# Kernel optimization log

Measured on AMD Instinct MI355X. Metric: run time of the kernel, lower is better.

## Reference

```python
import jax, jax.numpy as jnp
import numpy as np

S, B, D, H, A = 1024, 256, 128, 256, 256  # seq, batch, input_dim, hidden_dim, attention_dim


def setup_inputs() -> dict:
    key = jax.random.key(0)
    ks = jax.random.split(key, 8)
    sc_in = 1.0 / np.sqrt(D + H)
    sc_h = 1.0 / np.sqrt(H)
    inp = {
        "inputs": jax.random.normal(ks[0], (S, B, D), dtype=jnp.float32),
        "mask": jnp.ones((S, B), dtype=jnp.int32),
        "Wf": jax.random.uniform(ks[1], (D + H, H), jnp.float32, -sc_in, sc_in),
        "bf": jnp.zeros((H,), jnp.float32),
        "Wi": jax.random.uniform(ks[2], (D + H, H), jnp.float32, -sc_in, sc_in),
        "bi": jnp.zeros((H,), jnp.float32),
        "Wg": jax.random.uniform(ks[3], (D + H, H), jnp.float32, -sc_in, sc_in),
        "bg": jnp.zeros((H,), jnp.float32),
        "Wo": jax.random.uniform(ks[4], (D + H, H), jnp.float32, -sc_in, sc_in),
        "bo": jnp.zeros((H,), jnp.float32),
        "Wa": jax.random.uniform(ks[5], (H, A), jnp.float32, -sc_h, sc_h),
        "ba": jnp.zeros((A,), jnp.float32),
    }
    return inp


def reference(inputs, mask, Wf, bf, Wi, bi, Wg, bg, Wo, bo, Wa, ba):
    seq_len, batch, _ = inputs.shape
    h0 = jnp.zeros((batch, H), inputs.dtype)
    c0 = jnp.zeros((batch, H), inputs.dtype)
    mask_f = mask.astype(inputs.dtype)[:, :, None]  # (S, B, 1)

    def step(carry, xm):
        hx, cx = carry
        x_t, m_t = xm  # (B, D), (B, 1)
        combined = jnp.concatenate([x_t, hx], axis=1)  # (B, D+H)
        f = jax.nn.sigmoid(combined @ Wf + bf)
        i = jax.nn.sigmoid(combined @ Wi + bi)
        g = jnp.tanh(combined @ Wg + bg)
        o = jax.nn.sigmoid(combined @ Wo + bo)
        # masked gates: forget/output default to 1, input/update to 0 on padding
        f = f * m_t + (1.0 - m_t)
        i = i * m_t
        g = g * m_t
        o = o * m_t + (1.0 - m_t)
        cx = f * cx + i * g
        hx = o * jnp.tanh(cx)
        return (hx, cx), hx

    (hx, cx), outputs = jax.lax.scan(step, (h0, c0), (inputs, mask_f))  # outputs (S, B, H)

    # attention pooling over the time axis (dim 0); attention_dim == hidden_dim
    attn_weights = jax.nn.softmax(outputs @ Wa + ba, axis=0)  # (S, B, A)
    context = jnp.sum(attn_weights * outputs, axis=0)  # (B, H)
    outputs = jnp.broadcast_to(context[None, :, :], (seq_len, batch, H))
    return outputs, (hx, cx)
```

## Files before the change

### kernel.cpp

```cpp
#include <hip/hip_runtime.h>
#include <cstdint>
#include <cstddef>

#define WS_WHP   0
#define WS_WXP   524288
#define WS_WAP   786432
#define WS_CTX   917504
#define WS_XPROJ 1179648

typedef _Float16 h2_t __attribute__((ext_vector_type(2)));

static __device__ __forceinline__ float fdot2(uint32_t a, uint32_t b, float acc) {
#if __has_builtin(__builtin_amdgcn_fdot2)
    return __builtin_amdgcn_fdot2(__builtin_bit_cast(h2_t, a),
                                  __builtin_bit_cast(h2_t, b), acc, false);
#else
    union { uint32_t u; _Float16 f[2]; } ua, ub;
    ua.u = a; ub.u = b;
    return acc + (float)ua.f[0] * (float)ub.f[0] + (float)ua.f[1] * (float)ub.f[1];
#endif
}

static __device__ __forceinline__ uint32_t packh2(float x, float y) {
    h2_t v; v[0] = (_Float16)x; v[1] = (_Float16)y;
    return __builtin_bit_cast(uint32_t, v);
}
static __device__ __forceinline__ uint16_t f16b(float v) {
    _Float16 h = (_Float16)v; return __builtin_bit_cast(uint16_t, h);
}
static __device__ __forceinline__ float h16tof(uint16_t u) {
    return (float)__builtin_bit_cast(_Float16, u);
}
static __device__ __forceinline__ float sigm(float x) {
    return 1.0f / (1.0f + __expf(-x));
}
static __device__ __forceinline__ float tanh_fast(float x) {
    float ax = fabsf(x);
    float e = __expf(-2.0f * ax);
    float r = (1.0f - e) / (1.0f + e);
    return (x < 0.0f) ? -r : r;
}

__global__ void k_pack(const float* __restrict__ Wf, const float* __restrict__ Wi,
                       const float* __restrict__ Wg2, const float* __restrict__ Wo,
                       const float* __restrict__ Wa,
                       uint32_t* __restrict__ whp, uint32_t* __restrict__ wxp,
                       uint32_t* __restrict__ wap) {
    int idx = blockIdx.x * 256 + threadIdx.x;
    if (idx < 131072) {
        int p = idx >> 10, c = idx & 1023;
        int g = c >> 8, u = c & 255;
        const float* W = (g == 0) ? Wf : (g == 1) ? Wi : (g == 2) ? Wg2 : Wo;
        whp[idx] = packh2(W[(128 + 2 * p) * 256 + u], W[(129 + 2 * p) * 256 + u]);
    } else if (idx < 196608) {
        int j = idx - 131072;
        int p = j >> 10, c = j & 1023;
        int g = c >> 8, u = c & 255;
        const float* W = (g == 0) ? Wf : (g == 1) ? Wi : (g == 2) ? Wg2 : Wo;
        wxp[j] = packh2(W[(2 * p) * 256 + u], W[(2 * p + 1) * 256 + u]);
    } else if (idx < 229376) {
        int j = idx - 196608;
        int p = j >> 8, aa = j & 255;
        wap[j] = packh2(Wa[(2 * p) * 256 + aa], Wa[(2 * p + 1) * 256 + aa]);
    }
}

__global__ __launch_bounds__(512) void k_xproj(
        const float* __restrict__ x,
        const float* __restrict__ bfp, const float* __restrict__ bip,
        const float* __restrict__ bgp, const float* __restrict__ bop,
        const uint32_t* __restrict__ wxp, uint16_t* __restrict__ xproj) {
    __shared__ uint32_t xs[512];
    int t = threadIdx.x;
    int c0 = t, c1 = t + 512;
    uint32_t wx0[64], wx1[64];
#pragma unroll
    for (int p = 0; p < 64; ++p) {
        wx0[p] = wxp[p * 1024 + c0];
        wx1[p] = wxp[p * 1024 + c1];
    }
    float bias0 = (t < 256) ? bfp[t] : bip[t - 256];
    float bias1 = (t < 256) ? bgp[t] : bop[t - 256];
    int srow = t >> 6, pp = t & 63;
    long row0 = (long)blockIdx.x * 128;
    for (int ch = 0; ch < 16; ++ch) {
        long rbase = row0 + ch * 8;
        const float2* xr = (const float2*)(x + (rbase + srow) * 128) + pp;
        float2 xv = *xr;
        __syncthreads();
        xs[srow * 64 + pp] = packh2(xv.x, xv.y);
        __syncthreads();
#pragma unroll 1
        for (int r = 0; r < 8; ++r) {
            const uint32_t* hrow = xs + r * 64;
            float a0 = 0.f, d0 = 0.f, a1 = 0.f, d1 = 0.f;
#pragma unroll
            for (int p = 0; p < 64; p += 4) {
                uint4 hv = *(const uint4*)(hrow + p);
                a0 = fdot2(wx0[p + 0], hv.x, a0); d0 = fdot2(wx0[p + 1], hv.y, d0);
                a0 = fdot2(wx0[p + 2], hv.z, a0); d0 = fdot2(wx0[p + 3], hv.w, d0);
                a1 = fdot2(wx1[p + 0], hv.x, a1); d1 = fdot2(wx1[p + 1], hv.y, d1);
                a1 = fdot2(wx1[p + 2], hv.z, a1); d1 = fdot2(wx1[p + 3], hv.w, d1);
            }
            size_t orow = (size_t)(rbase + r) * 1024;
            xproj[orow + c0] = f16b(a0 + d0 + bias0);
            xproj[orow + c1] = f16b(a1 + d1 + bias1);
        }
    }
}

#define RECUR_LDS 152064

__global__ __launch_bounds__(512, 2) void k_recur(
        const uint32_t* __restrict__ whp, const uint16_t* __restrict__ xproj,
        const int* __restrict__ mask, uint16_t* __restrict__ oseq,
        float* __restrict__ dout) {
    extern __shared__ uint32_t smem[];
    uint32_t* wlds = smem;
    uint32_t* h2   = smem + 36864;
    float*    P    = (float*)(smem + 36992);
    int t = threadIdx.x;
    int b = blockIdx.x;
    int c0 = t, c1 = t + 512;

    for (int j = t; j < 32768; j += 512) {
        int c = j >> 5, pp = j & 31;
        wlds[c * 36 + pp] = whp[(96 + pp) * 1024 + c];
    }
    if (t < 128) h2[t] = 0u;

    uint32_t w0[96], w1[96];
#pragma unroll
    for (int p = 0; p < 96; ++p) {
        w0[p] = whp[p * 1024 + c0];
        w1[p] = whp[p * 1024 + c1];
    }
    float c_state = 0.f, h_state = 0.f;
    const uint16_t* xp_ptr = xproj + b * 1024;
    uint16_t* oseq_ptr = oseq + b * 256;
    uint16_t xv0 = xp_ptr[c0], xv1 = xp_ptr[c1];
    int mv = mask[b];
    __syncthreads();

    for (int s = 0; s < 1024; ++s) {
        float xpf0 = h16tof(xv0), xpf1 = h16tof(xv1);
        float mcur = (float)mv;
        xp_ptr += 262144;
        if (s < 1023) {
            xv0 = xp_ptr[c0]; xv1 = xp_ptr[c1];
            mv = mask[(s + 1) * 256 + b];
        }
        float a0 = 0.f, b0 = 0.f, a1 = 0.f, b1 = 0.f;
#pragma unroll
        for (int j = 0; j < 8; ++j) {
            uint4 hv = *(const uint4*)(h2 + 96 + j * 4);
            uint4 wA = *(const uint4*)(wlds + c0 * 36 + j * 4);
            uint4 wB = *(const uint4*)(wlds + c1 * 36 + j * 4);
            a0 = fdot2(wA.x, hv.x, a0); b0 = fdot2(wA.y, hv.y, b0);
            a0 = fdot2(wA.z, hv.z, a0); b0 = fdot2(wA.w, hv.w, b0);
            a1 = fdot2(wB.x, hv.x, a1); b1 = fdot2(wB.y, hv.y, b1);
            a1 = fdot2(wB.z, hv.z, a1); b1 = fdot2(wB.w, hv.w, b1);
        }
#pragma unroll
        for (int j = 0; j < 24; ++j) {
            uint4 hv = *(const uint4*)(h2 + j * 4);
            a0 = fdot2(w0[4 * j + 0], hv.x, a0); b0 = fdot2(w0[4 * j + 1], hv.y, b0);
            a0 = fdot2(w0[4 * j + 2], hv.z, a0); b0 = fdot2(w0[4 * j + 3], hv.w, b0);
            a1 = fdot2(w1[4 * j + 0], hv.x, a1); b1 = fdot2(w1[4 * j + 1], hv.y, b1);
            a1 = fdot2(w1[4 * j + 2], hv.z, a1); b1 = fdot2(w1[4 * j + 3], hv.w, b1);
        }
        P[c0] = a0 + b0 + xpf0;
        P[c1] = a1 + b1 + xpf1;
        __syncthreads();
        if (t < 256) {
            float fg = sigm(P[t]);
            float ig = sigm(P[256 + t]);
            float gg = tanh_fast(P[512 + t]);
            float og = sigm(P[768 + t]);
            fg = fg * mcur + (1.0f - mcur);
            ig = ig * mcur;
            gg = gg * mcur;
            og = og * mcur + (1.0f - mcur);
            c_state = fg * c_state + ig * gg;
            h_state = og * tanh_fast(c_state);
            uint16_t hb = f16b(h_state);
            ((uint16_t*)h2)[t] = hb;
            oseq_ptr[t] = hb;
        }
        __syncthreads();
        oseq_ptr += 65536;
    }
    if (t < 256) {
        dout[67108864 + b * 256 + t] = h_state;
        dout[67174400 + b * 256 + t] = c_state;
    }
}

__global__ __launch_bounds__(256) void k_attn(
        const uint32_t* __restrict__ wap, const float* __restrict__ ba,
        const uint16_t* __restrict__ oseq, float* __restrict__ ctx) {
    __shared__ uint32_t rb[2][128];
    int a = threadIdx.x, b = blockIdx.x;
    uint32_t wa[128];
#pragma unroll
    for (int p = 0; p < 128; ++p) wa[p] = wap[p * 256 + a];
    float bias = ba[a];
    const uint32_t* orow = (const uint32_t*)oseq + b * 128;
    if (a < 128) rb[0][a] = orow[a];
    __syncthreads();
    float m = -3.0e38f, Z = 0.f, acc = 0.f;
    for (int s = 0; s < 1024; ++s) {
        uint32_t nxt = 0;
        if (s < 1023 && a < 128) nxt = orow[32768 * (s + 1) + a];
        const uint32_t* row = rb[s & 1];
        float l0 = bias, l1 = 0.f, l2 = 0.f, l3 = 0.f;
#pragma unroll
        for (int p = 0; p < 128; p += 4) {
            uint4 hv = *(const uint4*)(row + p);
            l0 = fdot2(wa[p + 0], hv.x, l0);
            l1 = fdot2(wa[p + 1], hv.y, l1);
            l2 = fdot2(wa[p + 2], hv.z, l2);
            l3 = fdot2(wa[p + 3], hv.w, l3);
        }
        float l = (l0 + l1) + (l2 + l3);
        uint32_t pv = row[a >> 1];
        float hself = h16tof((a & 1) ? (uint16_t)(pv >> 16) : (uint16_t)(pv & 0xffffu));
        float m2 = fmaxf(m, l);
        float al = __expf(m - m2);
        float pr = __expf(l - m2);
        Z = Z * al + pr;
        acc = acc * al + pr * hself;
        m = m2;
        if (s < 1023 && a < 128) rb[(s + 1) & 1][a] = nxt;
        __syncthreads();
    }
    ctx[b * 256 + a] = acc / Z;
}

__global__ void k_bcast(const float4* __restrict__ ctx4, float4* __restrict__ out4) {
    int i = blockIdx.x * 256 + threadIdx.x;
    out4[i] = ctx4[i & 16383];
}

extern "C" void kernel_launch(void* const* d_in, const int* in_sizes, int n_in,
                              void* d_out, int out_size, void* d_ws, size_t ws_size,
                              hipStream_t stream) {
    const float* x    = (const float*)d_in[0];
    const int*   mask = (const int*)d_in[1];
    const float* Wf   = (const float*)d_in[2];
    const float* bf   = (const float*)d_in[3];
    const float* Wi   = (const float*)d_in[4];
    const float* bi   = (const float*)d_in[5];
    const float* Wg   = (const float*)d_in[6];
    const float* bg   = (const float*)d_in[7];
    const float* Wo   = (const float*)d_in[8];
    const float* bo   = (const float*)d_in[9];
    const float* Wa   = (const float*)d_in[10];
    const float* ba   = (const float*)d_in[11];
    float* out = (float*)d_out;
    char*  ws  = (char*)d_ws;

    uint32_t* whp   = (uint32_t*)(ws + WS_WHP);
    uint32_t* wxp   = (uint32_t*)(ws + WS_WXP);
    uint32_t* wap   = (uint32_t*)(ws + WS_WAP);
    float*    ctx   = (float*)(ws + WS_CTX);
    uint16_t* xproj = (uint16_t*)(ws + WS_XPROJ);
    uint16_t* oseq  = (uint16_t*)d_out;

    (void)in_sizes; (void)n_in; (void)out_size; (void)ws_size;

    hipFuncSetAttribute((const void*)k_recur,
                        hipFuncAttributeMaxDynamicSharedMemorySize, RECUR_LDS);

    k_pack<<<896, 256, 0, stream>>>(Wf, Wi, Wg, Wo, Wa, whp, wxp, wap);
    k_xproj<<<2048, 512, 0, stream>>>(x, bf, bi, bg, bo, wxp, xproj);
    k_recur<<<256, 512, RECUR_LDS, stream>>>(whp, xproj, mask, oseq, out);
    k_attn<<<256, 256, 0, stream>>>(wap, ba, oseq, ctx);
    k_bcast<<<65536, 256, 0, stream>>>((const float4*)ctx, (float4*)out);
}
```

Baseline: 3.866 ms.

## Restructure LSTM recurrence to one thread per hidden unit, split attention over time

The recurrent kernel now uses 256 threads, each computing all four gates for one hidden unit. Weights are split between registers (400 per thread) and LDS, and the hidden state is double-buffered, which removes one of the two barriers per step and the gate-exchange through shared memory. The attention pooling is split into four time chunks per batch, with partial max/sum/accumulator results merged by a new small kernel, so more blocks run in parallel. Risks are high register pressure from the 400-element weight arrays, which may cause spills, and fewer threads per CU during the serial recurrence.

```diff
diff --git a/kernel.cpp b/kernel.cpp
--- a/kernel.cpp
+++ b/kernel.cpp
@@ -109,109 +109,113 @@
     }
 }
 
-#define RECUR_LDS 152064
-
-__global__ __launch_bounds__(512, 2) void k_recur(
+#define RECUR_LDS 115712
+
+__global__ __launch_bounds__(256, 1) void k_recur(
         const uint32_t* __restrict__ whp, const uint16_t* __restrict__ xproj,
         const int* __restrict__ mask, uint16_t* __restrict__ oseq,
         float* __restrict__ dout) {
     extern __shared__ uint32_t smem[];
-    uint32_t* wlds = smem;
-    uint32_t* h2   = smem + 36864;
-    float*    P    = (float*)(smem + 36992);
+    uint32_t* wlds  = smem;
+    uint32_t* hbuf0 = smem + 28672;
+    uint32_t* hbuf1 = smem + 28800;
     int t = threadIdx.x;
     int b = blockIdx.x;
-    int c0 = t, c1 = t + 512;
-
-    for (int j = t; j < 32768; j += 512) {
-        int c = j >> 5, pp = j & 31;
-        wlds[c * 36 + pp] = whp[(96 + pp) * 1024 + c];
-    }
-    if (t < 128) h2[t] = 0u;
-
-    uint32_t w0[96], w1[96];
-#pragma unroll
-    for (int p = 0; p < 96; ++p) {
-        w0[p] = whp[p * 1024 + c0];
-        w1[p] = whp[p * 1024 + c1];
+
+    for (int p = 0; p < 28; ++p)
+        for (int c = t; c < 1024; c += 256)
+            wlds[c * 28 + p] = whp[(100 + p) * 1024 + c];
+    if (t < 128) hbuf0[t] = 0u;
+
+    uint32_t w0[100], w1[100], w2[100], w3[100];
+#pragma unroll
+    for (int p = 0; p < 100; ++p) {
+        const uint32_t* r = whp + p * 1024 + t;
+        w0[p] = r[0]; w1[p] = r[256]; w2[p] = r[512]; w3[p] = r[768];
     }
     float c_state = 0.f, h_state = 0.f;
-    const uint16_t* xp_ptr = xproj + b * 1024;
-    uint16_t* oseq_ptr = oseq + b * 256;
-    uint16_t xv0 = xp_ptr[c0], xv1 = xp_ptr[c1];
+    const uint16_t* xp = xproj + b * 1024 + t;
+    uint16_t* op = oseq + b * 256 + t;
+    uint16_t xf = xp[0], xi = xp[256], xg = xp[512], xo = xp[768];
     int mv = mask[b];
+    const uint32_t* wl = wlds + t * 28;
     __syncthreads();
 
     for (int s = 0; s < 1024; ++s) {
-        float xpf0 = h16tof(xv0), xpf1 = h16tof(xv1);
+        const uint32_t* hb = (s & 1) ? hbuf1 : hbuf0;
+        uint32_t*       hn = (s & 1) ? hbuf0 : hbuf1;
+        float pf = h16tof(xf), pi = h16tof(xi), pg = h16tof(xg), po = h16tof(xo);
         float mcur = (float)mv;
-        xp_ptr += 262144;
+        xp += 262144;
         if (s < 1023) {
-            xv0 = xp_ptr[c0]; xv1 = xp_ptr[c1];
+            xf = xp[0]; xi = xp[256]; xg = xp[512]; xo = xp[768];
             mv = mask[(s + 1) * 256 + b];
         }
-        float a0 = 0.f, b0 = 0.f, a1 = 0.f, b1 = 0.f;
-#pragma unroll
-        for (int j = 0; j < 8; ++j) {
-            uint4 hv = *(const uint4*)(h2 + 96 + j * 4);
-            uint4 wA = *(const uint4*)(wlds + c0 * 36 + j * 4);
-            uint4 wB = *(const uint4*)(wlds + c1 * 36 + j * 4);
-            a0 = fdot2(wA.x, hv.x, a0); b0 = fdot2(wA.y, hv.y, b0);
-            a0 = fdot2(wA.z, hv.z, a0); b0 = fdot2(wA.w, hv.w, b0);
-            a1 = fdot2(wB.x, hv.x, a1); b1 = fdot2(wB.y, hv.y, b1);
-            a1 = fdot2(wB.z, hv.z, a1); b1 = fdot2(wB.w, hv.w, b1);
-        }
-#pragma unroll
-        for (int j = 0; j < 24; ++j) {
-            uint4 hv = *(const uint4*)(h2 + j * 4);
-            a0 = fdot2(w0[4 * j + 0], hv.x, a0); b0 = fdot2(w0[4 * j + 1], hv.y, b0);
-            a0 = fdot2(w0[4 * j + 2], hv.z, a0); b0 = fdot2(w0[4 * j + 3], hv.w, b0);
-            a1 = fdot2(w1[4 * j + 0], hv.x, a1); b1 = fdot2(w1[4 * j + 1], hv.y, b1);
-            a1 = fdot2(w1[4 * j + 2], hv.z, a1); b1 = fdot2(w1[4 * j + 3], hv.w, b1);
-        }
-        P[c0] = a0 + b0 + xpf0;
-        P[c1] = a1 + b1 + xpf1;
+        float f0 = 0.f, f1 = 0.f, i0 = 0.f, i1 = 0.f;
+        float g0 = 0.f, g1 = 0.f, o0 = 0.f, o1 = 0.f;
+#pragma unroll
+        for (int j = 0; j < 7; ++j) {
+            uint4 hv = *(const uint4*)(hb + 100 + 4 * j);
+            uint4 wa = *(const uint4*)(wl + 4 * j);
+            uint4 wb = *(const uint4*)(wl + 7168 + 4 * j);
+            uint4 wc = *(const uint4*)(wl + 14336 + 4 * j);
+            uint4 wd = *(const uint4*)(wl + 21504 + 4 * j);
+            f0 = fdot2(wa.x, hv.x, f0); f1 = fdot2(wa.y, hv.y, f1);
+            f0 = fdot2(wa.z, hv.z, f0); f1 = fdot2(wa.w, hv.w, f1);
+            i0 = fdot2(wb.x, hv.x, i0); i1 = fdot2(wb.y, hv.y, i1);
+            i0 = fdot2(wb.z, hv.z, i0); i1 = fdot2(wb.w, hv.w, i1);
+            g0 = fdot2(wc.x, hv.x, g0); g1 = fdot2(wc.y, hv.y, g1);
+            g0 = fdot2(wc.z, hv.z, g0); g1 = fdot2(wc.w, hv.w, g1);
+            o0 = fdot2(wd.x, hv.x, o0); o1 = fdot2(wd.y, hv.y, o1);
+            o0 = fdot2(wd.z, hv.z, o0); o1 = fdot2(wd.w, hv.w, o1);
+        }
+#pragma unroll
+        for (int j = 0; j < 25; ++j) {
+            uint4 hv = *(const uint4*)(hb + 4 * j);
+            int p = 4 * j;
+            f0 = fdot2(w0[p + 0], hv.x, f0); f1 = fdot2(w0[p + 1], hv.y, f1);
+            f0 = fdot2(w0[p + 2], hv.z, f0); f1 = fdot2(w0[p + 3], hv.w, f1);
+            i0 = fdot2(w1[p + 0], hv.x, i0); i1 = fdot2(w1[p + 1], hv.y, i1);
+            i0 = fdot2(w1[p + 2], hv.z, i0); i1 = fdot2(w1[p + 3], hv.w, i1);
+            g0 = fdot2(w2[p + 0], hv.x, g0); g1 = fdot2(w2[p + 1], hv.y, g1);
+            g0 = fdot2(w2[p + 2], hv.z, g0); g1 = fdot2(w2[p + 3], hv.w, g1);
+            o0 = fdot2(w3[p + 0], hv.x, o0); o1 = fdot2(w3[p + 1], hv.y, o1);
+            o0 = fdot2(w3[p + 2], hv.z, o0); o1 = fdot2(w3[p + 3], hv.w, o1);
+        }
+        pf += f0 + f1; pi += i0 + i1; pg += g0 + g1; po += o0 + o1;
+        float fg = sigm(pf) * mcur + (1.0f - mcur);
+        float ig = sigm(pi) * mcur;
+        float gg = tanh_fast(pg) * mcur;
+        float og = sigm(po) * mcur + (1.0f - mcur);
+        c_state = fg * c_state + ig * gg;
+        h_state = og * tanh_fast(c_state);
+        uint16_t hbits = f16b(h_state);
+        ((uint16_t*)hn)[t] = hbits;
+        op[0] = hbits;
+        op += 65536;
         __syncthreads();
-        if (t < 256) {
-            float fg = sigm(P[t]);
-            float ig = sigm(P[256 + t]);
-            float gg = tanh_fast(P[512 + t]);
-            float og = sigm(P[768 + t]);
-            fg = fg * mcur + (1.0f - mcur);
-            ig = ig * mcur;
-            gg = gg * mcur;
-            og = og * mcur + (1.0f - mcur);
-            c_state = fg * c_state + ig * gg;
-            h_state = og * tanh_fast(c_state);
-            uint16_t hb = f16b(h_state);
-            ((uint16_t*)h2)[t] = hb;
-            oseq_ptr[t] = hb;
-        }
-        __syncthreads();
-        oseq_ptr += 65536;
-    }
-    if (t < 256) {
-        dout[67108864 + b * 256 + t] = h_state;
-        dout[67174400 + b * 256 + t] = c_state;
-    }
+    }
+    dout[67108864 + b * 256 + t] = h_state;
+    dout[67174400 + b * 256 + t] = c_state;
 }
 
 __global__ __launch_bounds__(256) void k_attn(
         const uint32_t* __restrict__ wap, const float* __restrict__ ba,
-        const uint16_t* __restrict__ oseq, float* __restrict__ ctx) {
+        const uint16_t* __restrict__ oseq, float* __restrict__ parts) {
     __shared__ uint32_t rb[2][128];
-    int a = threadIdx.x, b = blockIdx.x;
+    int a = threadIdx.x;
+    int b = blockIdx.x >> 2, ch = blockIdx.x & 3;
     uint32_t wa[128];
 #pragma unroll
     for (int p = 0; p < 128; ++p) wa[p] = wap[p * 256 + a];
     float bias = ba[a];
-    const uint32_t* orow = (const uint32_t*)oseq + b * 128;
+    const uint32_t* orow = (const uint32_t*)oseq + b * 128 + (size_t)ch * 256 * 32768;
     if (a < 128) rb[0][a] = orow[a];
     __syncthreads();
     float m = -3.0e38f, Z = 0.f, acc = 0.f;
-    for (int s = 0; s < 1024; ++s) {
+    for (int s = 0; s < 256; ++s) {
         uint32_t nxt = 0;
-        if (s < 1023 && a < 128) nxt = orow[32768 * (s + 1) + a];
+        if (s < 255 && a < 128) nxt = orow[32768 * (s + 1) + a];
         const uint32_t* row = rb[s & 1];
         float l0 = bias, l1 = 0.f, l2 = 0.f, l3 = 0.f;
 #pragma unroll
@@ -231,10 +235,35 @@
         Z = Z * al + pr;
         acc = acc * al + pr * hself;
         m = m2;
-        if (s < 1023 && a < 128) rb[(s + 1) & 1][a] = nxt;
+        if (s < 255 && a < 128) rb[(s + 1) & 1][a] = nxt;
         __syncthreads();
     }
-    ctx[b * 256 + a] = acc / Z;
+    int idx = ((b << 2) + ch) * 256 + a;
+    parts[idx] = m;
+    parts[262144 + idx] = Z;
+    parts[524288 + idx] = acc;
+}
+
+__global__ void k_attn2(const float* __restrict__ parts, float* __restrict__ ctx) {
+    int a = threadIdx.x, b = blockIdx.x;
+    float mv[4], zv[4], av[4];
+    float M = -3.0e38f;
+#pragma unroll
+    for (int c2 = 0; c2 < 4; ++c2) {
+        int idx = ((b << 2) + c2) * 256 + a;
+        mv[c2] = parts[idx];
+        zv[c2] = parts[262144 + idx];
+        av[c2] = parts[524288 + idx];
+        M = fmaxf(M, mv[c2]);
+    }
+    float Z = 0.f, A = 0.f;
+#pragma unroll
+    for (int c2 = 0; c2 < 4; ++c2) {
+        float e = __expf(mv[c2] - M);
+        Z += zv[c2] * e;
+        A += av[c2] * e;
+    }
+    ctx[b * 256 + a] = A / Z;
 }
 
 __global__ void k_bcast(const float4* __restrict__ ctx4, float4* __restrict__ out4) {
@@ -266,6 +295,7 @@
     float*    ctx   = (float*)(ws + WS_CTX);
     uint16_t* xproj = (uint16_t*)(ws + WS_XPROJ);
     uint16_t* oseq  = (uint16_t*)d_out;
+    float*    parts = (float*)d_out + 33554432;
 
     (void)in_sizes; (void)n_in; (void)out_size; (void)ws_size;
 
@@ -274,7 +304,8 @@
 
     k_pack<<<896, 256, 0, stream>>>(Wf, Wi, Wg, Wo, Wa, whp, wxp, wap);
     k_xproj<<<2048, 512, 0, stream>>>(x, bf, bi, bg, bo, wxp, xproj);
-    k_recur<<<256, 512, RECUR_LDS, stream>>>(whp, xproj, mask, oseq, out);
-    k_attn<<<256, 256, 0, stream>>>(wap, ba, oseq, ctx);
+    k_recur<<<256, 256, RECUR_LDS, stream>>>(whp, xproj, mask, oseq, out);
+    k_attn<<<1024, 256, 0, stream>>>(wap, ba, oseq, parts);
+    k_attn2<<<256, 256, 0, stream>>>(parts, ctx);
     k_bcast<<<65536, 256, 0, stream>>>((const float4*)ctx, (float4*)out);
 }
```

New measurement: 5.382 ms. 39.2% more time.
